# Performance work log

Hardware: AMD Instinct MI355X
Metric: run time of the kernel (lower is better)

The kernel has to match this reference:

```python
import jax, jax.numpy as jnp
import numpy as np

N, E, B, IN = 20000, 320000, 64, 192


def setup_inputs() -> dict:
    key = jax.random.key(0)
    ks = iter(jax.random.split(key, 80))
    d = {}
    d["x"] = jax.random.normal(next(ks), (N, IN), jnp.float32)
    d["edge_index"] = jax.random.randint(next(ks), (2, E), 0, N - 1)  # +1 shift stays < N
    d["edge_attr"] = jax.random.normal(next(ks), (E,), jnp.float32)
    d["batch"] = jnp.sort(jax.random.randint(next(ks), (N,), 0, B))

    def lin(i, o):
        w = jax.random.normal(next(ks), (i, o), jnp.float32) * (1.0 / i ** 0.5)
        return w, jnp.zeros((o,), jnp.float32)

    dims = [(IN, 4, 64), (256, 4, 64), (256, 6, 32)]  # (in_ch, heads, out_ch) per conv
    for l, (ic, h, c) in enumerate(dims, 1):
        hc = h * c
        d[f"Wq{l}"], d[f"bq{l}"] = lin(ic, hc)
        d[f"Wk{l}"], d[f"bk{l}"] = lin(ic, hc)
        d[f"Wv{l}"], d[f"bv{l}"] = lin(ic, hc)
        d[f"We{l}"] = jax.random.normal(next(ks), (1, hc), jnp.float32)  # lin_edge, no bias
        d[f"Ws{l}"], d[f"bs{l}"] = lin(ic, hc)  # root/skip weight
    d["g1"] = jnp.ones((256,), jnp.float32); d["be1"] = jnp.zeros((256,), jnp.float32)
    d["g2"] = jnp.ones((256,), jnp.float32); d["be2"] = jnp.zeros((256,), jnp.float32)
    d["fc1_w"], d["fc1_b"] = lin(192, 32)
    d["fc2_w"], d["fc2_b"] = lin(32, 2)
    return d


def seg_softmax(s, seg, n):
    # per-destination-node softmax over edges, [E, H]
    m = jax.ops.segment_max(s, seg, num_segments=n)
    m = jnp.where(jnp.isfinite(m), m, 0.0)
    ex = jnp.exp(s - m[seg])
    den = jax.ops.segment_sum(ex, seg, num_segments=n)
    return ex / (den[seg] + 1e-16)


def tconv(x, src, dst, e, Wq, bq, Wk, bk, Wv, bv, We, Ws, bs, h, c):
    # PyG TransformerConv (concat=True, root_weight=True, beta=False, eval -> no dropout)
    n = x.shape[0]
    q = (x @ Wq + bq).reshape(n, h, c)
    k = (x @ Wk + bk).reshape(n, h, c)
    v = (x @ Wv + bv).reshape(n, h, c)
    ee = (e @ We).reshape(-1, h, c)           # [E, h, c] edge embedding
    kj = k[src] + ee                           # gather keys along edges
    scores = jnp.einsum('ehc,ehc->eh', q[dst], kj) * (1.0 / c ** 0.5)
    alpha = seg_softmax(scores, dst, n)        # [E, h]
    msg = (v[src] + ee) * alpha[..., None]
    out = jax.ops.segment_sum(msg, dst, num_segments=n).reshape(n, h * c)
    return out + x @ Ws + bs, alpha


def ln(x, g, b):
    mu = x.mean(-1, keepdims=True)
    var = x.var(-1, keepdims=True)
    return g * (x - mu) / jnp.sqrt(var + 1e-5) + b


def _forward(x, edge_index, edge_attr, batch, Wq1, bq1, Wk1, bk1, Wv1, bv1, We1, Ws1, bs1, Wq2, bq2, Wk2, bk2, Wv2, bv2, We2, Ws2, bs2, Wq3, bq3, Wk3, bk3, Wv3, bv3, We3, Ws3, bs3, g1, be1, g2, be2, fc1_w, fc1_b, fc2_w, fc2_b):
    ei = edge_index + 1                       # replicates `edge_index += 1` in source
    src, dst = ei[0], ei[1]
    e = edge_attr[:, None]                    # edge_dim = 1
    x1, a1 = tconv(x, src, dst, e, Wq1, bq1, Wk1, bk1, Wv1, bv1, We1, Ws1, bs1, 4, 64)
    x1 = jax.nn.relu(ln(x1, g1, be1))
    x2, a2 = tconv(x1, src, dst, e, Wq2, bq2, Wk2, bk2, Wv2, bv2, We2, Ws2, bs2, 4, 64)
    x2 = jax.nn.relu(ln(x2, g2, be2))
    x3, a3 = tconv(x2, src, dst, e, Wq3, bq3, Wk3, bk3, Wv3, bv3, We3, Ws3, bs3, 6, 32)
    x3 = jax.nn.relu(x3)                      # note: norm3 exists in __init__ but is never applied
    xr = x + x3
    cnt = jax.ops.segment_sum(jnp.ones((xr.shape[0],), xr.dtype), batch, num_segments=B)
    pooled = jax.ops.segment_sum(xr, batch, num_segments=B) / jnp.maximum(cnt, 1.0)[:, None]
    h = jax.nn.relu(pooled @ fc1_w + fc1_b)
    logits = h @ fc2_w + fc2_b
    return logits, a1, a2, a3


def reference(x, edge_index, edge_attr, batch, Wq1, bq1, Wk1, bk1, Wv1, bv1, We1, Ws1, bs1, Wq2, bq2, Wk2, bk2, Wv2, bv2, We2, Ws2, bs2, Wq3, bq3, Wk3, bk3, Wv3, bv3, We3, Ws3, bs3, g1, be1, g2, be2, fc1_w, fc1_b, fc2_w, fc2_b):
    return _forward(x, edge_index, edge_attr, batch, Wq1, bq1, Wk1, bk1, Wv1, bv1, We1, Ws1, bs1, Wq2, bq2, Wk2, bk2, Wv2, bv2, We2, Ws2, bs2, Wq3, bq3, Wk3, bk3, Wv3, bv3, We3, Ws3, bs3, g1, be1, g2, be2, fc1_w, fc1_b, fc2_w, fc2_b)
```

## Files before the change

### kernel.cpp

```cpp
#include <hip/hip_runtime.h>
#include <cstdint>
#include <cstddef>

#define DEVINL __device__ __forceinline__

typedef short s16x8 __attribute__((ext_vector_type(8)));
typedef float f32x4 __attribute__((ext_vector_type(4)));
typedef unsigned short u16x4 __attribute__((ext_vector_type(4)));
typedef unsigned short u16x8 __attribute__((ext_vector_type(8)));

DEVINL unsigned short f2bf(float f) {
  unsigned u = __float_as_uint(f);
  unsigned r = (u + 0x7FFFu + ((u >> 16) & 1u)) >> 16;
  return (unsigned short)r;
}
DEVINL float bf2f(unsigned short b) { return __uint_as_float(((unsigned)b) << 16); }

__global__ __launch_bounds__(256) void fill_i32(int* __restrict__ p, int val, int n) {
  int i = blockIdx.x * 256 + threadIdx.x;
  if (i < n) p[i] = val;
}


__global__ __launch_bounds__(256) void cvt_split(const float* __restrict__ in,
                                                 unsigned short* __restrict__ hi,
                                                 unsigned short* __restrict__ lo, int n) {
  int i = blockIdx.x * 256 + threadIdx.x;
  if (i >= n) return;
  float f = in[i];
  unsigned short h = f2bf(f);
  float r = f - bf2f(h);
  hi[i] = h;
  lo[i] = f2bf(r);
}

struct CvtWArgs {
  const float* W[12];
  int K[12];
  int M[12];
};
__global__ __launch_bounds__(256) void cvt_w_all(CvtWArgs a,
                                                 unsigned short* __restrict__ Wh,
                                                 unsigned short* __restrict__ Wl) {
  int tid = blockIdx.x * 256 + threadIdx.x;
  int mat = tid >> 16;
  int off = tid & 65535;
  if (mat >= 12) return;
  int K = a.K[mat], M = a.M[mat];
  if (off >= K * M) return;
  int k = off / M, m = off - k * M;
  float f = a.W[mat][off];
  unsigned short h = f2bf(f);
  float r = f - bf2f(h);
  size_t dst = (size_t)mat * 65536 + (size_t)m * K + k;
  Wh[dst] = h;
  Wl[dst] = f2bf(r);
}

struct GemmArgs {
  const unsigned short* Wh[4];
  const unsigned short* Wl[4];
  const float* bias[4];
  float* out[4];
  int obf[4];
};

template <int KTOT>
__global__ __launch_bounds__(256, 3) void gemm4_lds(
    const unsigned short* __restrict__ Ah, const unsigned short* __restrict__ Al,
    GemmArgs args, int N, int M) {
  const int BK = 64;
  __shared__ unsigned short ash[128 * 64];
  __shared__ unsigned short asl[128 * 64];
  __shared__ unsigned short wsh[64 * 64];
  __shared__ unsigned short wsl[64 * 64];
  int tid = threadIdx.x;
  int wave = tid >> 6, lane = tid & 63;
  int lrow = lane & 15, quad = lane >> 4;
  int mt = M >> 6;
  int ntile = mt * 4;
  int id = blockIdx.x, nwg = gridDim.x;
  int q8 = nwg >> 3, r8 = nwg & 7;
  int xcd = id & 7, j8 = id >> 3;
  int wg = (xcd < r8 ? xcd * (q8 + 1) : r8 * (q8 + 1) + (xcd - r8) * q8) + j8;
  int by = wg / ntile;
  int bxx = wg - by * ntile;
  int z = bxx / mt;
  int colTile = bxx - z * mt;
  int row0 = by * 128;
  int col0 = colTile * 64;
  const unsigned short* __restrict__ Wh = args.Wh[z];
  const unsigned short* __restrict__ Wl = args.Wl[z];
  const bool full = (args.obf[z] == 0);

  int ar[4], asq[4];
  size_t agoff[4];
#pragma unroll
  for (int i = 0; i < 4; i++) {
    int c = tid + i * 256;
    ar[i] = c >> 3;
    int kq = c & 7;
    asq[i] = kq ^ (ar[i] & 7);
    int gr = row0 + ar[i]; if (gr >= N) gr = N - 1;
    agoff[i] = (size_t)gr * KTOT + kq * 8;
  }
  int wr[2], wsq[2];
  size_t wgoff[2];
#pragma unroll
  for (int i = 0; i < 2; i++) {
    int c = tid + i * 256;
    wr[i] = c >> 3;
    int kq = c & 7;
    wsq[i] = kq ^ (wr[i] & 7);
    wgoff[i] = (size_t)(col0 + wr[i]) * KTOT + kq * 8;
  }

  s16x8 pa_h[4], pa_l[4], pw_h[2], pw_l[2];
#pragma unroll
  for (int i = 0; i < 4; i++) {
    pa_h[i] = *(const s16x8*)(Ah + agoff[i]);
    pa_l[i] = *(const s16x8*)(Al + agoff[i]);
  }
#pragma unroll
  for (int i = 0; i < 2; i++) {
    pw_h[i] = *(const s16x8*)(Wh + wgoff[i]);
    if (full) pw_l[i] = *(const s16x8*)(Wl + wgoff[i]);
  }

  f32x4 acc[2][4] = {};

  for (int k0 = 0; k0 < KTOT; k0 += BK) {
    __syncthreads();
#pragma unroll
    for (int i = 0; i < 4; i++) {
      *(s16x8*)(ash + ar[i] * 64 + asq[i] * 8) = pa_h[i];
      *(s16x8*)(asl + ar[i] * 64 + asq[i] * 8) = pa_l[i];
    }
#pragma unroll
    for (int i = 0; i < 2; i++) {
      *(s16x8*)(wsh + wr[i] * 64 + wsq[i] * 8) = pw_h[i];
      if (full) *(s16x8*)(wsl + wr[i] * 64 + wsq[i] * 8) = pw_l[i];
    }
    if (k0 + BK < KTOT) {
      int kn = k0 + BK;
#pragma unroll
      for (int i = 0; i < 4; i++) {
        pa_h[i] = *(const s16x8*)(Ah + agoff[i] + kn);
        pa_l[i] = *(const s16x8*)(Al + agoff[i] + kn);
      }
#pragma unroll
      for (int i = 0; i < 2; i++) {
        pw_h[i] = *(const s16x8*)(Wh + wgoff[i] + kn);
        if (full) pw_l[i] = *(const s16x8*)(Wl + wgoff[i] + kn);
      }
    }
    __syncthreads();
#pragma unroll
    for (int kk = 0; kk < 2; kk++) {
      s16x8 fah[2], fal[2], fbh[4], fbl[4];
#pragma unroll
      for (int rf = 0; rf < 2; rf++) {
        int r = wave * 32 + rf * 16 + lrow;
        int sq = (kk * 4 + quad) ^ (lrow & 7);
        fah[rf] = *(const s16x8*)(ash + r * 64 + sq * 8);
        fal[rf] = *(const s16x8*)(asl + r * 64 + sq * 8);
      }
#pragma unroll
      for (int cf = 0; cf < 4; cf++) {
        int cc = cf * 16 + lrow;
        int sq = (kk * 4 + quad) ^ (lrow & 7);
        fbh[cf] = *(const s16x8*)(wsh + cc * 64 + sq * 8);
        if (full) fbl[cf] = *(const s16x8*)(wsl + cc * 64 + sq * 8);
      }
#pragma unroll
      for (int rf = 0; rf < 2; rf++)
#pragma unroll
        for (int cf = 0; cf < 4; cf++) {
          acc[rf][cf] = __builtin_amdgcn_mfma_f32_16x16x32_bf16(fah[rf], fbh[cf], acc[rf][cf], 0, 0, 0);
          acc[rf][cf] = __builtin_amdgcn_mfma_f32_16x16x32_bf16(fal[rf], fbh[cf], acc[rf][cf], 0, 0, 0);
          if (full)
            acc[rf][cf] = __builtin_amdgcn_mfma_f32_16x16x32_bf16(fah[rf], fbl[cf], acc[rf][cf], 0, 0, 0);
        }
    }
  }
  const float* __restrict__ bias = args.bias[z];
  int obf = args.obf[z];
  if (obf == 0) {
    float* __restrict__ C = args.out[z];
#pragma unroll
    for (int cf = 0; cf < 4; cf++) {
      int col = col0 + cf * 16 + lrow;
      float bv = bias[col];
#pragma unroll
      for (int rf = 0; rf < 2; rf++) {
        int rb = row0 + wave * 32 + rf * 16 + quad * 4;
#pragma unroll
        for (int r = 0; r < 4; r++) {
          int rr = rb + r;
          if (rr < N) C[(size_t)rr * M + col] = acc[rf][cf][r] + bv;
        }
      }
    }
  } else {
    __syncthreads();
#pragma unroll
    for (int cf = 0; cf < 4; cf++) {
      int col = cf * 16 + lrow;
      float bv = bias[col0 + col];
#pragma unroll
      for (int rf = 0; rf < 2; rf++) {
        int rl = wave * 32 + rf * 16 + quad * 4;
#pragma unroll
        for (int r = 0; r < 4; r++)
          ash[(rl + r) * 64 + col] = f2bf(acc[rf][cf][r] + bv);
      }
    }
    __syncthreads();
    unsigned short* __restrict__ C = (unsigned short*)args.out[z];
#pragma unroll
    for (int i = 0; i < 4; i++) {
      int c = tid + i * 256;
      int row = c >> 3, g8 = c & 7;
      int rr = row0 + row;
      if (rr < N)
        *(u16x8*)(C + (size_t)rr * M + col0 + g8 * 8) =
            *(const u16x8*)(ash + row * 64 + g8 * 8);
    }
  }
}


__global__ __launch_bounds__(256) void hist_dst(const int* __restrict__ dst,
                                                int* __restrict__ cnt, int E) {
  int e = blockIdx.x * 256 + threadIdx.x;
  if (e < E) atomicAdd(&cnt[dst[e] + 1], 1);
}

__global__ __launch_bounds__(1024) void scan_hist(const int* __restrict__ cnt,
                                                  int* __restrict__ start,
                                                  int* __restrict__ off, int N) {
  __shared__ int sums[1024];
  const int CH = 20;
  int t = threadIdx.x;
  int base = t * CH;
  int local[CH];
  int tot = 0;
  if (base < N) {
#pragma unroll
    for (int i = 0; i < CH; i++) { local[i] = cnt[base + i]; tot += local[i]; }
  }
  sums[t] = tot;
  __syncthreads();
  for (int d = 1; d < 1024; d <<= 1) {
    int v = (t >= d) ? sums[t - d] : 0;
    __syncthreads();
    sums[t] += v;
    __syncthreads();
  }
  if (base < N) {
    int run = (t == 0) ? 0 : sums[t - 1];
#pragma unroll
    for (int i = 0; i < CH; i++) { start[base + i] = run; off[base + i] = run; run += local[i]; }
    if (base + CH == N) start[N] = run;
  }
}

__global__ __launch_bounds__(256) void scatter_edges(
    const int* __restrict__ src, const int* __restrict__ dst,
    const float* __restrict__ ea, int* __restrict__ off,
    int* __restrict__ src_s, float* __restrict__ ea_s, int* __restrict__ eid_s, int E) {
  int e = blockIdx.x * 256 + threadIdx.x;
  if (e >= E) return;
  int d = dst[e] + 1;
  int pos = atomicAdd(&off[d], 1);
  src_s[pos] = src[e] + 1;
  ea_s[pos] = ea[e];
  eid_s[pos] = e;
}

template <int H, int ACT, int MODE>
__global__ __launch_bounds__(256) void attn_fused(
    const unsigned short* __restrict__ q, const unsigned short* __restrict__ kb,
    const unsigned short* __restrict__ vb, const float* __restrict__ We,
    const int* __restrict__ start, const int* __restrict__ src_s,
    const float* __restrict__ ea_s, const int* __restrict__ eid_s,
    float* __restrict__ sc, float* __restrict__ outp,
    float* __restrict__ alpha, int Nn, float scale,
    const float* __restrict__ gam, const float* __restrict__ bet,
    unsigned short* __restrict__ hi, unsigned short* __restrict__ lo) {
  const int HC = ACT * 8;
  const int LPH2 = ACT / H;
  int w = (blockIdx.x * 256 + threadIdx.x) >> 6;
  int lane = threadIdx.x & 63;
  if (w >= Nn) return;
  int b = start[w], e = start[w + 1];
  int hlane = lane & 31, half = lane >> 5;
  bool act = hlane < ACT;
  int idx = hlane * 8;
  int head = hlane / LPH2;
  float q8[8], We8[8];
#pragma unroll
  for (int j = 0; j < 8; j++) { q8[j] = 0.f; We8[j] = 0.f; }
  if (act) {
    u16x8 qv = *(const u16x8*)(q + (size_t)w * HC + idx);
#pragma unroll
    for (int j = 0; j < 8; j++) q8[j] = bf2f(qv[j]);
    float4 w0 = *(const float4*)(We + idx);
    float4 w1 = *(const float4*)(We + idx + 4);
    We8[0] = w0.x; We8[1] = w0.y; We8[2] = w0.z; We8[3] = w0.w;
    We8[4] = w1.x; We8[5] = w1.y; We8[6] = w1.z; We8[7] = w1.w;
  }
  float qwe = 0.f;
#pragma unroll
  for (int j = 0; j < 8; j++) qwe = fmaf(q8[j], We8[j], qwe);
#pragma unroll
  for (int mm = 1; mm < LPH2; mm <<= 1) qwe += __shfl_xor(qwe, mm, 64);

  float l = 0.f, tv = 0.f;
  float accv[8] = {0.f, 0.f, 0.f, 0.f, 0.f, 0.f, 0.f, 0.f};

  auto step = [&](u16x8 kc, u16x8 vc, float eav, int pairpos) {
    bool vld = (pairpos + half) < e;
    float p = 0.f;
#pragma unroll
    for (int j = 0; j < 8; j++) p = fmaf(q8[j], bf2f(kc[j]), p);
#pragma unroll
    for (int mm = 1; mm < LPH2; mm <<= 1) p += __shfl_xor(p, mm, 64);
    float es = __expf((p + eav * qwe) * scale);
    if (!vld) es = 0.f;
    if (act && vld && (hlane % LPH2) == 0)
      sc[(size_t)(pairpos + half) * H + head] = es;
    l += es;
    tv = fmaf(es, eav, tv);
#pragma unroll
    for (int j = 0; j < 8; j++) accv[j] = fmaf(es, bf2f(vc[j]), accv[j]);
  };

  u16x8 z8 = {0, 0, 0, 0, 0, 0, 0, 0};
  u16x8 kS[4] = {z8, z8, z8, z8};
  u16x8 vS[4] = {z8, z8, z8, z8};
  float eaS[4] = {0.f, 0.f, 0.f, 0.f};

  auto preload = [&](int pairpos, int st) {
    int pp = pairpos + half;
    int pc = pp < e ? pp : (e - 1);
    int s = src_s[pc];
    eaS[st] = ea_s[pc];
    if (act) {
      kS[st] = *(const u16x8*)(kb + (size_t)s * HC + idx);
      vS[st] = *(const u16x8*)(vb + (size_t)s * HC + idx);
    }
  };

#pragma unroll
  for (int j = 0; j < 4; j++) if (b + 2 * j < e) preload(b + 2 * j, j);

  for (int pos = b; pos < e; pos += 8) {
#pragma unroll
    for (int j = 0; j < 4; j++) {
      int pp = pos + 2 * j;
      if (pp < e) {
        u16x8 kc = kS[j];
        u16x8 vc = vS[j];
        float ec = eaS[j];
        if (pp + 8 < e) preload(pp + 8, j);
        step(kc, vc, ec, pp);
      }
    }
  }

  l += __shfl_xor(l, 32, 64);
  tv += __shfl_xor(tv, 32, 64);
#pragma unroll
  for (int j = 0; j < 8; j++) accv[j] += __shfl_xor(accv[j], 32, 64);

  float invl = 1.0f / (l + 1e-16f);
  if (MODE == 1) {
    if (half == 0) {
      const float* orow = outp + (size_t)w * HC + idx;
      float4 o0 = *(const float4*)orow;
      float4 o1 = *(const float4*)(orow + 4);
      float y[8] = {o0.x, o0.y, o0.z, o0.w, o1.x, o1.y, o1.z, o1.w};
#pragma unroll
      for (int j = 0; j < 8; j++) y[j] += (accv[j] + tv * We8[j]) * invl;
      float s = 0.f, s2 = 0.f;
#pragma unroll
      for (int j = 0; j < 8; j++) { s += y[j]; s2 = fmaf(y[j], y[j], s2); }
#pragma unroll
      for (int mm = 1; mm < 32; mm <<= 1) {
        s += __shfl_xor(s, mm, 64);
        s2 += __shfl_xor(s2, mm, 64);
      }
      float mu = s * (1.0f / 256.0f);
      float var = s2 * (1.0f / 256.0f) - mu * mu;
      float rinv = rsqrtf(var + 1e-5f);
      float4 g0 = *(const float4*)(gam + idx);
      float4 g1v = *(const float4*)(gam + idx + 4);
      float4 b0 = *(const float4*)(bet + idx);
      float4 b1 = *(const float4*)(bet + idx + 4);
      float gg[8] = {g0.x, g0.y, g0.z, g0.w, g1v.x, g1v.y, g1v.z, g1v.w};
      float bb[8] = {b0.x, b0.y, b0.z, b0.w, b1.x, b1.y, b1.z, b1.w};
      u16x8 yh, yl;
#pragma unroll
      for (int j = 0; j < 8; j++) {
        float t = fmaxf(fmaf((y[j] - mu) * rinv, gg[j], bb[j]), 0.f);
        unsigned short hh = f2bf(t);
        yh[j] = hh;
        yl[j] = f2bf(t - bf2f(hh));
      }
      *(u16x8*)(hi + (size_t)w * HC + idx) = yh;
      *(u16x8*)(lo + (size_t)w * HC + idx) = yl;
    }
  } else {
    if (act && half == 0) {
      float* orow = outp + (size_t)w * HC + idx;
      float4 o0 = *(float4*)orow;
      float4 o1 = *(float4*)(orow + 4);
      o0.x += (accv[0] + tv * We8[0]) * invl;
      o0.y += (accv[1] + tv * We8[1]) * invl;
      o0.z += (accv[2] + tv * We8[2]) * invl;
      o0.w += (accv[3] + tv * We8[3]) * invl;
      o1.x += (accv[4] + tv * We8[4]) * invl;
      o1.y += (accv[5] + tv * We8[5]) * invl;
      o1.z += (accv[6] + tv * We8[6]) * invl;
      o1.w += (accv[7] + tv * We8[7]) * invl;
      *(float4*)orow = o0;
      *(float4*)(orow + 4) = o1;
    }
  }
  {
    int len = e - b;
    const int PCH = 64 / H;
    int p_of = lane / H;
    int h_of = lane - p_of * H;
    float myinv = __shfl(invl, h_of * LPH2, 64);
    __threadfence_block();
    for (int base = 0; base < len; base += PCH) {
      int po = base + p_of;
      if (p_of < PCH && po < len) {
        int pos = b + po;
        float es = sc[(size_t)pos * H + h_of];
        alpha[(size_t)eid_s[pos] * H + h_of] = es * myinv;
      }
    }
  }
}


__global__ __launch_bounds__(192) void resid_pool2(
    const float* __restrict__ x, const float* __restrict__ x3,
    const int* __restrict__ batch, float* __restrict__ pooled,
    float* __restrict__ cnt, int N, int R) {
  int col = threadIdx.x;
  int r0 = blockIdx.x * R;
  int r1 = min(r0 + R, N);
  if (r0 >= N) return;
  float acc = 0.f;
  int cur = batch[r0];
  int run = 0;
  for (int r = r0; r < r1; r++) {
    int b = batch[r];
    if (b != cur) {
      atomicAdd(&pooled[cur * 192 + col], acc);
      if (col == 0) atomicAdd(&cnt[cur], (float)run);
      acc = 0.f; run = 0; cur = b;
    }
    size_t i = (size_t)r * 192 + col;
    acc += x[i] + fmaxf(x3[i], 0.f);
    run++;
  }
  atomicAdd(&pooled[cur * 192 + col], acc);
  if (col == 0) atomicAdd(&cnt[cur], (float)run);
}

__global__ __launch_bounds__(64) void head_mlp(
    const float* __restrict__ pooled, const float* __restrict__ cnt,
    const float* __restrict__ fc1w, const float* __restrict__ fc1b,
    const float* __restrict__ fc2w, const float* __restrict__ fc2b,
    float* __restrict__ logits) {
  int b = blockIdx.x;
  int t = threadIdx.x;
  __shared__ float p[192];
  __shared__ float hbuf[32];
  float inv = 1.0f / fmaxf(cnt[b], 1.0f);
  for (int i = t; i < 192; i += 64) p[i] = pooled[b * 192 + i] * inv;
  __syncthreads();
  if (t < 32) {
    float acc = fc1b[t];
    for (int i = 0; i < 192; i++) acc = fmaf(p[i], fc1w[i * 32 + t], acc);
    hbuf[t] = fmaxf(acc, 0.f);
  }
  __syncthreads();
  if (t < 2) {
    float acc = fc2b[t];
    for (int j = 0; j < 32; j++) acc = fmaf(hbuf[j], fc2w[j * 2 + t], acc);
    logits[b * 2 + t] = acc;
  }
}

static inline int divup(int a, int b) { return (a + b - 1) / b; }

extern "C" void kernel_launch(void* const* d_in, const int* in_sizes, int n_in,
                              void* d_out, int out_size, void* d_ws, size_t ws_size,
                              hipStream_t stream) {
  const int N = 20000, E = 320000, B = 64;
  const float* x     = (const float*)d_in[0];
  const int*   ei    = (const int*)d_in[1];
  const float* eattr = (const float*)d_in[2];
  const int*   batch = (const int*)d_in[3];
  const int* srcp = ei;
  const int* dstp = ei + E;

  const float* Wq[3]; const float* bq[3]; const float* Wk[3]; const float* bk[3];
  const float* Wv[3]; const float* bv[3]; const float* We[3]; const float* Ws[3];
  const float* bs[3];
  for (int l = 0; l < 3; l++) {
    int base = 4 + l * 9;
    Wq[l] = (const float*)d_in[base + 0]; bq[l] = (const float*)d_in[base + 1];
    Wk[l] = (const float*)d_in[base + 2]; bk[l] = (const float*)d_in[base + 3];
    Wv[l] = (const float*)d_in[base + 4]; bv[l] = (const float*)d_in[base + 5];
    We[l] = (const float*)d_in[base + 6];
    Ws[l] = (const float*)d_in[base + 7]; bs[l] = (const float*)d_in[base + 8];
  }
  const float* g1  = (const float*)d_in[31]; const float* be1 = (const float*)d_in[32];
  const float* g2  = (const float*)d_in[33]; const float* be2 = (const float*)d_in[34];
  const float* fc1w = (const float*)d_in[35]; const float* fc1b = (const float*)d_in[36];
  const float* fc2w = (const float*)d_in[37]; const float* fc2b = (const float*)d_in[38];

  float* out = (float*)d_out;
  float* logits = out;
  float* a1 = out + 128;
  float* a2 = a1 + (size_t)E * 4;
  float* a3 = a2 + (size_t)E * 4;

  float* ws = (float*)d_ws;
  size_t o = 0;
  float* qb = ws + o; o += (size_t)N * 256;
  float* kvb = ws + o; o += (size_t)N * 256;
  float* xa = ws + o; o += (size_t)N * 256;
  float* xb = ws + o; o += (size_t)N * 256;
  float* sc = ws + o; o += (size_t)E * 6;
  int*   cntb  = (int*)(ws + o); o += N;
  int*   startb= (int*)(ws + o); o += N + 1;
  int*   offb  = (int*)(ws + o); o += N + 1;
  int*   src_s = (int*)(ws + o); o += E;
  float* ea_s  = ws + o; o += E;
  int*   eid_s = (int*)(ws + o); o += E;
  float* pooled = ws + o; o += (size_t)B * 192;
  float* cnt    = ws + o; o += B;
  unsigned short* Ah = (unsigned short*)(ws + o); o += (size_t)N * 128;
  unsigned short* Al = (unsigned short*)(ws + o); o += (size_t)N * 128;
  unsigned short* Wh12 = (unsigned short*)(ws + o); o += (size_t)12 * 32768;
  unsigned short* Wl12 = (unsigned short*)(ws + o); o += (size_t)12 * 32768;

  unsigned short* qh = (unsigned short*)qb;
  unsigned short* kh = (unsigned short*)kvb;
  unsigned short* vh = kh + (size_t)N * 256;

  dim3 blk(256);

  struct LayerCfg { int K, M; float scale; };
  LayerCfg cfg[3] = {
    {192, 256, 0.125f},
    {256, 256, 0.125f},
    {256, 192, 0.1767766952966369f},
  };
  CvtWArgs cwa;
  for (int l = 0; l < 3; l++) {
    cwa.W[l * 4 + 0] = Wq[l]; cwa.W[l * 4 + 1] = Wk[l];
    cwa.W[l * 4 + 2] = Wv[l]; cwa.W[l * 4 + 3] = Ws[l];
    for (int zz = 0; zz < 4; zz++) {
      cwa.K[l * 4 + zz] = cfg[l].K; cwa.M[l * 4 + zz] = cfg[l].M;
    }
  }
  cvt_w_all<<<12 * 65536 / 256, blk, 0, stream>>>(cwa, Wh12, Wl12);

  fill_i32<<<divup(N, 256), blk, 0, stream>>>(cntb, 0, N);
  hist_dst<<<divup(E, 256), blk, 0, stream>>>(dstp, cntb, E);
  scan_hist<<<1, dim3(1024), 0, stream>>>(cntb, startb, offb, N);
  scatter_edges<<<divup(E, 256), blk, 0, stream>>>(srcp, dstp, eattr, offb,
                                                  src_s, ea_s, eid_s, E);

  float*       lay_out[3] = {xb, xb, xa};
  float*       alpha_out[3] = {a1, a2, a3};
  const float* gams[3] = {g1, g2, nullptr};
  const float* bets[3] = {be1, be2, nullptr};

  cvt_split<<<divup(N * 192, 256), blk, 0, stream>>>(x, Ah, Al, N * 192);

  int stripes = divup(N, 128);
  for (int l = 0; l < 3; l++) {
    int M = cfg[l].M;
    GemmArgs ga;
    float* outs[4] = {(float*)qh, (float*)kh, (float*)vh, lay_out[l]};
    const float* biases[4] = {bq[l], bk[l], bv[l], bs[l]};
    int obfs[4] = {1, 1, 1, 0};
    for (int z = 0; z < 4; z++) {
      ga.Wh[z] = Wh12 + (size_t)(l * 4 + z) * 65536;
      ga.Wl[z] = Wl12 + (size_t)(l * 4 + z) * 65536;
      ga.bias[z] = biases[z];
      ga.out[z] = outs[z];
      ga.obf[z] = obfs[z];
    }
    dim3 gg((M >> 6) * 4 * stripes);
    if (l == 0)      gemm4_lds<192><<<gg, blk, 0, stream>>>(Ah, Al, ga, N, M);
    else             gemm4_lds<256><<<gg, blk, 0, stream>>>(Ah, Al, ga, N, M);

    dim3 gat(divup(N * 64, 256));
    if (l < 2) {
      attn_fused<4, 32, 1><<<gat, blk, 0, stream>>>(
          qh, kh, vh, We[l], startb, src_s, ea_s, eid_s, sc, lay_out[l],
          alpha_out[l], N, cfg[l].scale, gams[l], bets[l], Ah, Al);
    } else {
      attn_fused<6, 24, 0><<<gat, blk, 0, stream>>>(
          qh, kh, vh, We[l], startb, src_s, ea_s, eid_s, sc, lay_out[l],
          alpha_out[l], N, cfg[l].scale, nullptr, nullptr, nullptr, nullptr);
    }
  }

  fill_i32<<<divup(B * 192 + B, 256), blk, 0, stream>>>((int*)pooled, 0, B * 192 + B);
  resid_pool2<<<divup(N, 32), dim3(192), 0, stream>>>(x, xa, batch, pooled, cnt, N, 32);
  head_mlp<<<B, dim3(64), 0, stream>>>(pooled, cnt, fc1w, fc1b, fc2w, fc2b, logits);
}
```

Before: 576.8 us.

## Load GEMM operands directly from global memory and fuse layer-1 input split

Replaces the LDS-staged, register-prefetched GEMM with a version where each wave loads its MFMA fragments straight from global memory, keeping LDS only for the bf16 output staging, and raises the occupancy hint to four blocks. For layer 1 it reads fp32 x directly and performs the hi/lo bf16 split inside the GEMM, removing the separate cvt_split kernel and its write-then-read of the split arrays. The cost is that operands are no longer shared through LDS: each wave refetches the weight tile and each A row is reloaded by every column-tile block, and for layer 1 the split is recomputed per load. This puts more load on L2/global bandwidth and drops the software prefetch that overlapped loads with compute.

```diff
diff --git a/kernel.cpp b/kernel.cpp
--- a/kernel.cpp
+++ b/kernel.cpp
@@ -19,19 +19,6 @@
 __global__ __launch_bounds__(256) void fill_i32(int* __restrict__ p, int val, int n) {
   int i = blockIdx.x * 256 + threadIdx.x;
   if (i < n) p[i] = val;
-}
-
-
-__global__ __launch_bounds__(256) void cvt_split(const float* __restrict__ in,
-                                                 unsigned short* __restrict__ hi,
-                                                 unsigned short* __restrict__ lo, int n) {
-  int i = blockIdx.x * 256 + threadIdx.x;
-  if (i >= n) return;
-  float f = in[i];
-  unsigned short h = f2bf(f);
-  float r = f - bf2f(h);
-  hi[i] = h;
-  lo[i] = f2bf(r);
 }
 
 struct CvtWArgs {
@@ -65,15 +52,11 @@
   int obf[4];
 };
 
-template <int KTOT>
-__global__ __launch_bounds__(256, 3) void gemm4_lds(
+template <int KTOT, int F32A>
+__global__ __launch_bounds__(256, 4) void gemm4_direct(
     const unsigned short* __restrict__ Ah, const unsigned short* __restrict__ Al,
-    GemmArgs args, int N, int M) {
-  const int BK = 64;
-  __shared__ unsigned short ash[128 * 64];
-  __shared__ unsigned short asl[128 * 64];
-  __shared__ unsigned short wsh[64 * 64];
-  __shared__ unsigned short wsl[64 * 64];
+    const float* __restrict__ Af, GemmArgs args, int N, int M) {
+  __shared__ unsigned short cst[128 * 64];
   int tid = threadIdx.x;
   int wave = tid >> 6, lane = tid & 63;
   int lrow = lane & 15, quad = lane >> 4;
@@ -93,84 +76,44 @@
   const unsigned short* __restrict__ Wl = args.Wl[z];
   const bool full = (args.obf[z] == 0);
 
-  int ar[4], asq[4];
-  size_t agoff[4];
-#pragma unroll
-  for (int i = 0; i < 4; i++) {
-    int c = tid + i * 256;
-    ar[i] = c >> 3;
-    int kq = c & 7;
-    asq[i] = kq ^ (ar[i] & 7);
-    int gr = row0 + ar[i]; if (gr >= N) gr = N - 1;
-    agoff[i] = (size_t)gr * KTOT + kq * 8;
-  }
-  int wr[2], wsq[2];
-  size_t wgoff[2];
-#pragma unroll
-  for (int i = 0; i < 2; i++) {
-    int c = tid + i * 256;
-    wr[i] = c >> 3;
-    int kq = c & 7;
-    wsq[i] = kq ^ (wr[i] & 7);
-    wgoff[i] = (size_t)(col0 + wr[i]) * KTOT + kq * 8;
-  }
-
-  s16x8 pa_h[4], pa_l[4], pw_h[2], pw_l[2];
-#pragma unroll
-  for (int i = 0; i < 4; i++) {
-    pa_h[i] = *(const s16x8*)(Ah + agoff[i]);
-    pa_l[i] = *(const s16x8*)(Al + agoff[i]);
-  }
-#pragma unroll
-  for (int i = 0; i < 2; i++) {
-    pw_h[i] = *(const s16x8*)(Wh + wgoff[i]);
-    if (full) pw_l[i] = *(const s16x8*)(Wl + wgoff[i]);
+  int rA[2];
+#pragma unroll
+  for (int rf = 0; rf < 2; rf++) {
+    int r = row0 + wave * 32 + rf * 16 + lrow;
+    rA[rf] = (r < N) ? r : (N - 1);
   }
 
   f32x4 acc[2][4] = {};
 
-  for (int k0 = 0; k0 < KTOT; k0 += BK) {
-    __syncthreads();
-#pragma unroll
-    for (int i = 0; i < 4; i++) {
-      *(s16x8*)(ash + ar[i] * 64 + asq[i] * 8) = pa_h[i];
-      *(s16x8*)(asl + ar[i] * 64 + asq[i] * 8) = pa_l[i];
-    }
-#pragma unroll
-    for (int i = 0; i < 2; i++) {
-      *(s16x8*)(wsh + wr[i] * 64 + wsq[i] * 8) = pw_h[i];
-      if (full) *(s16x8*)(wsl + wr[i] * 64 + wsq[i] * 8) = pw_l[i];
-    }
-    if (k0 + BK < KTOT) {
-      int kn = k0 + BK;
-#pragma unroll
-      for (int i = 0; i < 4; i++) {
-        pa_h[i] = *(const s16x8*)(Ah + agoff[i] + kn);
-        pa_l[i] = *(const s16x8*)(Al + agoff[i] + kn);
-      }
-#pragma unroll
-      for (int i = 0; i < 2; i++) {
-        pw_h[i] = *(const s16x8*)(Wh + wgoff[i] + kn);
-        if (full) pw_l[i] = *(const s16x8*)(Wl + wgoff[i] + kn);
-      }
-    }
-    __syncthreads();
+  for (int k0 = 0; k0 < KTOT; k0 += 64) {
 #pragma unroll
     for (int kk = 0; kk < 2; kk++) {
+      int kcol = k0 + kk * 32 + quad * 8;
       s16x8 fah[2], fal[2], fbh[4], fbl[4];
 #pragma unroll
       for (int rf = 0; rf < 2; rf++) {
-        int r = wave * 32 + rf * 16 + lrow;
-        int sq = (kk * 4 + quad) ^ (lrow & 7);
-        fah[rf] = *(const s16x8*)(ash + r * 64 + sq * 8);
-        fal[rf] = *(const s16x8*)(asl + r * 64 + sq * 8);
+        if (F32A) {
+          const float* ap = Af + (size_t)rA[rf] * KTOT + kcol;
+          float4 a0 = *(const float4*)ap;
+          float4 a1 = *(const float4*)(ap + 4);
+          float av[8] = {a0.x, a0.y, a0.z, a0.w, a1.x, a1.y, a1.z, a1.w};
+#pragma unroll
+          for (int j = 0; j < 8; j++) {
+            unsigned short h = f2bf(av[j]);
+            fah[rf][j] = (short)h;
+            fal[rf][j] = (short)f2bf(av[j] - bf2f(h));
+          }
+        } else {
+          size_t ao = (size_t)rA[rf] * KTOT + kcol;
+          fah[rf] = *(const s16x8*)(Ah + ao);
+          fal[rf] = *(const s16x8*)(Al + ao);
+        }
       }
 #pragma unroll
       for (int cf = 0; cf < 4; cf++) {
-        int cc = cf * 16 + lrow;
-        int sq = (kk * 4 + quad) ^ (lrow & 7);
-        fbh[cf] = *(const s16x8*)(wsh + cc * 64 + sq * 8);
-        if (full) fbl[cf] = *(const s16x8*)(wsl + cc * 64 + sq * 8);
+        size_t wo = (size_t)(col0 + cf * 16 + lrow) * KTOT + kcol;
+        fbh[cf] = *(const s16x8*)(Wh + wo);
+        if (full) fbl[cf] = *(const s16x8*)(Wl + wo);
       }
 #pragma unroll
       for (int rf = 0; rf < 2; rf++)
@@ -212,7 +155,7 @@
         int rl = wave * 32 + rf * 16 + quad * 4;
 #pragma unroll
         for (int r = 0; r < 4; r++)
-          ash[(rl + r) * 64 + col] = f2bf(acc[rf][cf][r] + bv);
+          cst[(rl + r) * 64 + col] = f2bf(acc[rf][cf][r] + bv);
       }
     }
     __syncthreads();
@@ -224,7 +167,7 @@
       int rr = row0 + row;
       if (rr < N)
         *(u16x8*)(C + (size_t)rr * M + col0 + g8 * 8) =
-            *(const u16x8*)(ash + row * 64 + g8 * 8);
+            *(const u16x8*)(cst + row * 64 + g8 * 8);
     }
   }
 }
@@ -586,8 +529,6 @@
   const float* gams[3] = {g1, g2, nullptr};
   const float* bets[3] = {be1, be2, nullptr};
 
-  cvt_split<<<divup(N * 192, 256), blk, 0, stream>>>(x, Ah, Al, N * 192);
-
   int stripes = divup(N, 128);
   for (int l = 0; l < 3; l++) {
     int M = cfg[l].M;
@@ -603,8 +544,10 @@
       ga.obf[z] = obfs[z];
     }
     dim3 gg((M >> 6) * 4 * stripes);
-    if (l == 0)      gemm4_lds<192><<<gg, blk, 0, stream>>>(Ah, Al, ga, N, M);
-    else             gemm4_lds<256><<<gg, blk, 0, stream>>>(Ah, Al, ga, N, M);
+    if (l == 0)
+      gemm4_direct<192, 1><<<gg, blk, 0, stream>>>(Ah, Al, x, ga, N, M);
+    else
+      gemm4_direct<256, 0><<<gg, blk, 0, stream>>>(Ah, Al, nullptr, ga, N, M);
 
     dim3 gat(divup(N * 64, 256));
     if (l < 2) {
```

Result: slower. 686.1 us (+18.9%).

## Fuse fp32 input split into first GEMM and read low weight fragments from global

Applied to the files above, without the earlier changes.

Removes the separate cvt_split kernel and instead has layer-1 GEMM load fp32 x directly and split it into bf16 hi/lo in registers. It also drops the LDS buffer for the low-part weights, loading those fragments straight from global memory inside the MFMA loop, and raises the occupancy hint from 3 to 4 blocks. This cuts one kernel launch and an intermediate round trip through memory, and reduces LDS use. In exchange it adds uncached-in-LDS global loads in the inner loop and more conversion ALU work per tile.

```diff
diff --git a/kernel.cpp b/kernel.cpp
--- a/kernel.cpp
+++ b/kernel.cpp
@@ -19,19 +19,6 @@
 __global__ __launch_bounds__(256) void fill_i32(int* __restrict__ p, int val, int n) {
   int i = blockIdx.x * 256 + threadIdx.x;
   if (i < n) p[i] = val;
-}
-
-
-__global__ __launch_bounds__(256) void cvt_split(const float* __restrict__ in,
-                                                 unsigned short* __restrict__ hi,
-                                                 unsigned short* __restrict__ lo, int n) {
-  int i = blockIdx.x * 256 + threadIdx.x;
-  if (i >= n) return;
-  float f = in[i];
-  unsigned short h = f2bf(f);
-  float r = f - bf2f(h);
-  hi[i] = h;
-  lo[i] = f2bf(r);
 }
 
 struct CvtWArgs {
@@ -65,15 +52,14 @@
   int obf[4];
 };
 
-template <int KTOT>
-__global__ __launch_bounds__(256, 3) void gemm4_lds(
+template <int KTOT, int F32A>
+__global__ __launch_bounds__(256, 4) void gemm4_lds(
     const unsigned short* __restrict__ Ah, const unsigned short* __restrict__ Al,
-    GemmArgs args, int N, int M) {
+    const float* __restrict__ Af, GemmArgs args, int N, int M) {
   const int BK = 64;
   __shared__ unsigned short ash[128 * 64];
   __shared__ unsigned short asl[128 * 64];
   __shared__ unsigned short wsh[64 * 64];
-  __shared__ unsigned short wsl[64 * 64];
   int tid = threadIdx.x;
   int wave = tid >> 6, lane = tid & 63;
   int lrow = lane & 15, quad = lane >> 4;
@@ -115,17 +101,29 @@
     wgoff[i] = (size_t)(col0 + wr[i]) * KTOT + kq * 8;
   }
 
-  s16x8 pa_h[4], pa_l[4], pw_h[2], pw_l[2];
-#pragma unroll
-  for (int i = 0; i < 4; i++) {
-    pa_h[i] = *(const s16x8*)(Ah + agoff[i]);
-    pa_l[i] = *(const s16x8*)(Al + agoff[i]);
-  }
-#pragma unroll
-  for (int i = 0; i < 2; i++) {
-    pw_h[i] = *(const s16x8*)(Wh + wgoff[i]);
-    if (full) pw_l[i] = *(const s16x8*)(Wl + wgoff[i]);
-  }
+  auto loadA = [&](int i, int kn, s16x8& ph, s16x8& pl) {
+    if (F32A) {
+      const float* ap = Af + agoff[i] + kn;
+      float4 a0 = *(const float4*)ap;
+      float4 a1 = *(const float4*)(ap + 4);
+      float av[8] = {a0.x, a0.y, a0.z, a0.w, a1.x, a1.y, a1.z, a1.w};
+#pragma unroll
+      for (int j = 0; j < 8; j++) {
+        unsigned short h = f2bf(av[j]);
+        ph[j] = (short)h;
+        pl[j] = (short)f2bf(av[j] - bf2f(h));
+      }
+    } else {
+      ph = *(const s16x8*)(Ah + agoff[i] + kn);
+      pl = *(const s16x8*)(Al + agoff[i] + kn);
+    }
+  };
+
+  s16x8 pa_h[4], pa_l[4], pw_h[2];
+#pragma unroll
+  for (int i = 0; i < 4; i++) loadA(i, 0, pa_h[i], pa_l[i]);
+#pragma unroll
+  for (int i = 0; i < 2; i++) pw_h[i] = *(const s16x8*)(Wh + wgoff[i]);
 
   f32x4 acc[2][4] = {};
 
@@ -137,22 +135,15 @@
       *(s16x8*)(asl + ar[i] * 64 + asq[i] * 8) = pa_l[i];
     }
 #pragma unroll
-    for (int i = 0; i < 2; i++) {
+    for (int i = 0; i < 2; i++)
       *(s16x8*)(wsh + wr[i] * 64 + wsq[i] * 8) = pw_h[i];
-      if (full) *(s16x8*)(wsl + wr[i] * 64 + wsq[i] * 8) = pw_l[i];
-    }
     if (k0 + BK < KTOT) {
       int kn = k0 + BK;
 #pragma unroll
-      for (int i = 0; i < 4; i++) {
-        pa_h[i] = *(const s16x8*)(Ah + agoff[i] + kn);
-        pa_l[i] = *(const s16x8*)(Al + agoff[i] + kn);
-      }
-#pragma unroll
-      for (int i = 0; i < 2; i++) {
+      for (int i = 0; i < 4; i++) loadA(i, kn, pa_h[i], pa_l[i]);
+#pragma unroll
+      for (int i = 0; i < 2; i++)
         pw_h[i] = *(const s16x8*)(Wh + wgoff[i] + kn);
-        if (full) pw_l[i] = *(const s16x8*)(Wl + wgoff[i] + kn);
-      }
     }
     __syncthreads();
 #pragma unroll
@@ -165,12 +156,14 @@
         fah[rf] = *(const s16x8*)(ash + r * 64 + sq * 8);
         fal[rf] = *(const s16x8*)(asl + r * 64 + sq * 8);
       }
+      int kcol = k0 + kk * 32 + quad * 8;
 #pragma unroll
       for (int cf = 0; cf < 4; cf++) {
         int cc = cf * 16 + lrow;
         int sq = (kk * 4 + quad) ^ (lrow & 7);
         fbh[cf] = *(const s16x8*)(wsh + cc * 64 + sq * 8);
-        if (full) fbl[cf] = *(const s16x8*)(wsl + cc * 64 + sq * 8);
+        if (full)
+          fbl[cf] = *(const s16x8*)(Wl + (size_t)(col0 + cc) * KTOT + kcol);
       }
 #pragma unroll
       for (int rf = 0; rf < 2; rf++)
@@ -586,8 +579,6 @@
   const float* gams[3] = {g1, g2, nullptr};
   const float* bets[3] = {be1, be2, nullptr};
 
-  cvt_split<<<divup(N * 192, 256), blk, 0, stream>>>(x, Ah, Al, N * 192);
-
   int stripes = divup(N, 128);
   for (int l = 0; l < 3; l++) {
     int M = cfg[l].M;
@@ -603,8 +594,10 @@
       ga.obf[z] = obfs[z];
     }
     dim3 gg((M >> 6) * 4 * stripes);
-    if (l == 0)      gemm4_lds<192><<<gg, blk, 0, stream>>>(Ah, Al, ga, N, M);
-    else             gemm4_lds<256><<<gg, blk, 0, stream>>>(Ah, Al, ga, N, M);
+    if (l == 0)
+      gemm4_lds<192, 1><<<gg, blk, 0, stream>>>(Ah, Al, x, ga, N, M);
+    else
+      gemm4_lds<256, 0><<<gg, blk, 0, stream>>>(Ah, Al, nullptr, ga, N, M);
 
     dim3 gat(divup(N * 64, 256));
     if (l < 2) {
```

Measured after the change: 835.3 us. 44.8% more time.
